# Performance work log

Measured on AMD Instinct MI355X. Metric: run time of the kernel, lower is better.

The kernel has to match this reference:

```python
import jax, jax.numpy as jnp
import numpy as np

N = 100000   # nodes
E = 800000   # directed edges
G = 1000     # graphs
D = 128      # latent_dim
F_IN = 64    # num_node_feats
K = 3        # max_k
BLOCKS = 3   # max_block
H = 5        # multi_h_emb_weight
EPS = 1e-5


def _bn(x, g, b):
    # BatchNorm1d in training mode: biased batch variance
    m = x.mean(axis=0)
    v = x.var(axis=0)
    return (x - m) * jax.lax.rsqrt(v + EPS) * g + b


def setup_inputs() -> dict:
    key = jax.random.key(0)
    ks = jax.random.split(key, 12)
    inp = {
        'node_feat': jax.random.normal(ks[0], (N, F_IN), dtype=jnp.float32),
        'src': jax.random.randint(ks[1], (E,), 0, N),
        'dst': jax.random.randint(ks[2], (E,), 0, N),
        'seg': jnp.sort(jax.random.randint(ks[3], (N,), 0, G)),
        'node_W': jax.random.normal(ks[4], (F_IN, D), dtype=jnp.float32) * 0.05,
        'node_b': jnp.zeros((D,), jnp.float32),
        'bn1_g': jnp.ones((D,), jnp.float32),
        'bn1_b': jnp.zeros((D,), jnp.float32),
        'conv_W': jax.random.normal(ks[5], (K, D, D), dtype=jnp.float32) * 0.05,
        'conv_b': jnp.zeros((K, D), jnp.float32),
        'bn2_g': jnp.ones((K, D), jnp.float32),
        'bn2_b': jnp.zeros((K, D), jnp.float32),
        'k_weight': jax.random.normal(ks[6], (K * D, D), dtype=jnp.float32) * 0.05,
        'bn3_g': jnp.ones((D,), jnp.float32),
        'bn3_b': jnp.zeros((D,), jnp.float32),
        'attn_W1': jax.random.normal(ks[7], (D, D), dtype=jnp.float32) * 0.05,
        'attn_b1': jnp.zeros((D,), jnp.float32),
        'bna_g': jnp.ones((D,), jnp.float32),
        'bna_b': jnp.zeros((D,), jnp.float32),
        'attn_W2': jax.random.normal(ks[8], (D, H), dtype=jnp.float32) * 0.05,
        'attn_b2': jnp.zeros((H,), jnp.float32),
        'bnb_g': jnp.ones((H,), jnp.float32),
        'bnb_b': jnp.zeros((H,), jnp.float32),
    }
    return inp


def reference(node_feat, src, dst, seg,
              node_W, node_b, bn1_g, bn1_b,
              conv_W, conv_b, bn2_g, bn2_b,
              k_weight, bn3_g, bn3_b,
              attn_W1, attn_b1, bna_g, bna_b,
              attn_W2, attn_b2, bnb_g, bnb_b):
    def spmm(x):
        # torch.spmm(A, x) with unweighted n2n adjacency: out[dst] += x[src]
        return jax.ops.segment_sum(x[src], dst, num_segments=N)

    # node embedding: Linear + BN + ReLU
    inp = jax.nn.relu(_bn(node_feat @ node_W + node_b, bn1_g, bn1_b))

    cur = inp
    for block in range(BLOCKS):
        block_input = cur if block == 0 else cur + inp
        # multi_hop: K chained spmm + Linear + BN, concatenated
        input_x = block_input
        outs = []
        for k in range(K):
            pooled = spmm(input_x) + block_input
            input_x = _bn(pooled @ conv_W[k] + conv_b[k], bn2_g[k], bn2_b[k])
            outs.append(input_x)
        result = jnp.concatenate(outs, axis=-1)          # [N, K*D]
        cur = jax.nn.relu(_bn(result @ k_weight, bn3_g, bn3_b))

    node_emb = cur                                       # [N, D]

    # APooling: per-node softmax over heads, segment-wise weighted sum
    a = jnp.tanh(node_emb @ attn_W1 + attn_b1)
    a = _bn(a, bna_g, bna_b)
    a = a @ attn_W2 + attn_b2
    a = _bn(a, bnb_g, bnb_b)                             # [N, H]
    alpha = jax.nn.softmax(a, axis=-1)                   # softmax over head dim (dim=-1)
    # graph_emb[g, h, d] = sum_{n in graph g} alpha[n, h] * node_emb[n, d]
    graph_emb = jax.ops.segment_sum(alpha[:, :, None] * node_emb[:, None, :],
                                    seg, num_segments=G)  # [G, H, D]
    h_out = jax.nn.relu(graph_emb.reshape(G, H * D))

    # L1 regularizer over params with dim > 1, divided by number of graphs
    reg = (jnp.abs(node_W).sum() + jnp.abs(conv_W).sum() + jnp.abs(k_weight).sum()
           + jnp.abs(attn_W1).sum() + jnp.abs(attn_W2).sum())
    return h_out, reg / G
```

## Files before the change

### kernel.cpp

```cpp
#include <hip/hip_runtime.h>
#include <hip/hip_bf16.h>

#define D128 128
#define EPS 1e-5f

typedef unsigned short bfl;
typedef __bf16 bf16x8 __attribute__((ext_vector_type(8)));
typedef float f32x4 __attribute__((ext_vector_type(4)));

__device__ inline float bf2f(unsigned short u) { return __uint_as_float(((unsigned int)u) << 16); }
__device__ inline unsigned short f2bf(float f) {
    unsigned int x = __float_as_uint(f);
    return (unsigned short)((x + 0x7fffu + ((x >> 16) & 1u)) >> 16);
}

__global__ void dag_count_rank(const int* __restrict__ dst, int E,
                               int* __restrict__ deg, int* __restrict__ rank) {
    int i = blockIdx.x * blockDim.x + threadIdx.x;
    int stride = gridDim.x * blockDim.x;
    for (; i < E; i += stride) {
        int r = atomicAdd(&deg[dst[i]], 1);
        rank[i] = r;
    }
}

__global__ void dag_scan1(const int* __restrict__ deg, int N, int* __restrict__ out, int* __restrict__ partials) {
    __shared__ int sdata[256];
    int t = threadIdx.x;
    int base = blockIdx.x * 1024 + t * 4;
    int v[4]; int s = 0;
#pragma unroll
    for (int j = 0; j < 4; j++) { int idx = base + j; v[j] = (idx < N) ? deg[idx] : 0; s += v[j]; }
    sdata[t] = s; __syncthreads();
    for (int off = 1; off < 256; off <<= 1) {
        int x = (t >= off) ? sdata[t - off] : 0;
        __syncthreads();
        sdata[t] += x;
        __syncthreads();
    }
    int run = (t == 0) ? 0 : sdata[t - 1];
#pragma unroll
    for (int j = 0; j < 4; j++) { int idx = base + j; if (idx < N) out[idx] = run; run += v[j]; }
    if (t == 255) partials[blockIdx.x] = sdata[255];
}

__global__ void dag_scan2(int* __restrict__ partials, int P) {
    __shared__ int sdata[256];
    int t = threadIdx.x;
    int v = (t < P) ? partials[t] : 0;
    sdata[t] = v; __syncthreads();
    for (int off = 1; off < 256; off <<= 1) {
        int x = (t >= off) ? sdata[t - off] : 0;
        __syncthreads();
        sdata[t] += x;
        __syncthreads();
    }
    if (t < P) partials[t] = sdata[t] - v;
}

__global__ void dag_scan3(int* __restrict__ rowptr, const int* __restrict__ partials, int N, int E) {
    int i = blockIdx.x * blockDim.x + threadIdx.x;
    int stride = gridDim.x * blockDim.x;
    for (; i < N; i += stride) rowptr[i] += partials[i >> 10];
    if (blockIdx.x == 0 && threadIdx.x == 0) rowptr[N] = E;
}

__global__ void dag_place(const int* __restrict__ src, const int* __restrict__ dst,
                          const int* __restrict__ rank, const int* __restrict__ rowptr,
                          int E, int* __restrict__ csr_src) {
    int i = blockIdx.x * blockDim.x + threadIdx.x;
    int stride = gridDim.x * blockDim.x;
    for (; i < E; i += stride) {
        csr_src[rowptr[dst[i]] + rank[i]] = src[i];
    }
}

__global__ void dag_wconv(const float* __restrict__ node_W, const float* __restrict__ conv_W,
                          const float* __restrict__ k_weight, const float* __restrict__ attn_W1,
                          bfl* __restrict__ wt) {
    int i = blockIdx.x * blockDim.x + threadIdx.x;
    if (i >= 122880) return;
    float v;
    if (i < 8192) {
        int n = i >> 6, k = i & 63;
        v = node_W[k * 128 + n];
    } else if (i < 8192 + 49152) {
        int j = i - 8192; int k = j >> 14; int r = j & 16383;
        int n = r >> 7, kk = r & 127;
        v = conv_W[k * 16384 + kk * 128 + n];
    } else if (i < 8192 + 98304) {
        int j = i - 8192 - 49152; int k = j >> 14; int r = j & 16383;
        int n = r >> 7, kk = r & 127;
        v = k_weight[(k * 128 + kk) * 128 + n];
    } else {
        int j = i - 8192 - 98304;
        int n = j >> 7, kk = j & 127;
        v = attn_W1[kk * 128 + n];
    }
    wt[i] = f2bf(v);
}

template<bool KWPREP>
__global__ void dag_finalize(float* __restrict__ part,
                             const float* __restrict__ g, const float* __restrict__ b,
                             float invN, float* __restrict__ slot,
                             const bfl* __restrict__ WtIn, bfl* __restrict__ Wt2,
                             float* __restrict__ bias2) {
    int t = threadIdx.x;
    float acc = 0.f;
#pragma unroll
    for (int i = 0; i < 8; i++) acc += part[i * 256 + t];
#pragma unroll
    for (int i = 0; i < 8; i++) part[i * 256 + t] = 0.f;
    __shared__ float sums[256];
    __shared__ float scs[128], shs[128];
    sums[t] = acc;
    __syncthreads();
    if (t < 128) {
        float m = sums[t] * invN;
        float var = sums[128 + t] * invN - m * m;
        float scale = g[t] * rsqrtf(var + EPS);
        float shift = b[t] - m * scale;
        scs[t] = scale; shs[t] = shift;
        slot[t] = scale; slot[128 + t] = shift;
    }
    if constexpr (KWPREP) {
        __syncthreads();
        int row = t >> 1, half = t & 1;
        const bfl* wr = WtIn + row * 128 + half * 64;
        bfl* w2 = Wt2 + row * 128 + half * 64;
        float a = 0.f;
        for (int k = 0; k < 64; k += 8) {
            bf16x8 v = *(const bf16x8*)(wr + k);
            bfl o[8];
#pragma unroll
            for (int j = 0; j < 8; j++) {
                float f = (float)v[j];
                int kk = half * 64 + k + j;
                a += shs[kk] * f;
                o[j] = f2bf(scs[kk] * f);
            }
            *(bf16x8*)(w2 + k) = *(bf16x8*)o;
        }
        a += __shfl_xor(a, 1);
        if (half == 0) bias2[row] = a;
    }
}

template<int KSTEPS, int XMODE, bool BIAS, bool TANH, bool ACC, bool STATS>
__global__ __launch_bounds__(256) void gemm_rw(
        const void* __restrict__ Xv, const bfl* __restrict__ Wt,
        const float* __restrict__ bias, bfl* __restrict__ Y,
        int Nrows, float* __restrict__ partOut) {
    const int Kdim = KSTEPS * 32;
    int t = threadIdx.x;
    int lane = t & 63;
    int wave = t >> 6;
    int cg = wave & 1, rg = wave >> 1;
    int l15 = lane & 15, lg = lane >> 4;

    bf16x8 af[4][KSTEPS];
#pragma unroll
    for (int nf = 0; nf < 4; nf++)
#pragma unroll
        for (int ks = 0; ks < KSTEPS; ks++)
            af[nf][ks] = *(const bf16x8*)(Wt + (size_t)(cg * 64 + nf * 16 + l15) * Kdim + ks * 32 + lg * 8);

    float bia[4][4];
    if (BIAS) {
#pragma unroll
        for (int nf = 0; nf < 4; nf++) {
            float4 bb = *(const float4*)(bias + cg * 64 + nf * 16 + lg * 4);
            bia[nf][0] = bb.x; bia[nf][1] = bb.y; bia[nf][2] = bb.z; bia[nf][3] = bb.w;
        }
    }

    float s_c[4][4], q_c[4][4];
    if constexpr (STATS) {
#pragma unroll
        for (int nf = 0; nf < 4; nf++)
#pragma unroll
            for (int j = 0; j < 4; j++) { s_c[nf][j] = 0.f; q_c[nf][j] = 0.f; }
    }

    const int RT = (Nrows + 15) >> 4;
    const int step = gridDim.x * 2;

    auto load_bf = [&](int rt, bf16x8* bfo) {
        int r = rt * 16 + l15;
        bool valid = (rt < RT) && (r < Nrows);
#pragma unroll
        for (int ks = 0; ks < KSTEPS; ks++) {
            if (valid) {
                if (XMODE == 0) {
                    bfo[ks] = *(const bf16x8*)((const bfl*)Xv + (size_t)r * Kdim + ks * 32 + lg * 8);
                } else {
                    const float* xp = (const float*)Xv + (size_t)r * Kdim + ks * 32 + lg * 8;
                    float4 a4 = *(const float4*)xp;
                    float4 b4 = *(const float4*)(xp + 4);
                    bf16x8 bb;
                    bb[0] = (__bf16)a4.x; bb[1] = (__bf16)a4.y; bb[2] = (__bf16)a4.z; bb[3] = (__bf16)a4.w;
                    bb[4] = (__bf16)b4.x; bb[5] = (__bf16)b4.y; bb[6] = (__bf16)b4.z; bb[7] = (__bf16)b4.w;
                    bfo[ks] = bb;
                }
            } else {
                bf16x8 bb;
#pragma unroll
                for (int j = 0; j < 8; j++) bb[j] = (__bf16)0.f;
                bfo[ks] = bb;
            }
        }
    };

    auto compute_store = [&](int rt, const bf16x8* bfc) {
        int r = rt * 16 + l15;
        bool valid = (rt < RT) && (r < Nrows);
        f32x4 acc[4];
#pragma unroll
        for (int nf = 0; nf < 4; nf++) acc[nf] = (f32x4)0.f;
#pragma unroll
        for (int ks = 0; ks < KSTEPS; ks++)
#pragma unroll
            for (int nf = 0; nf < 4; nf++)
                acc[nf] = __builtin_amdgcn_mfma_f32_16x16x32_bf16(af[nf][ks], bfc[ks], acc[nf], 0, 0, 0);
#pragma unroll
        for (int nf = 0; nf < 4; nf++) {
            int c0 = cg * 64 + nf * 16 + lg * 4;
            f32x4 v = acc[nf];
            if (BIAS) {
#pragma unroll
                for (int j = 0; j < 4; j++) v[j] += bia[nf][j];
            }
            if (TANH) {
#pragma unroll
                for (int j = 0; j < 4; j++) v[j] = tanhf(v[j]);
            }
            if (valid) {
                bfl* yp = Y + (size_t)r * D128 + c0;
                if (ACC) {
                    ushort4 old = *(const ushort4*)yp;
                    v[0] += bf2f(old.x); v[1] += bf2f(old.y); v[2] += bf2f(old.z); v[3] += bf2f(old.w);
                }
                ushort4 o;
                o.x = f2bf(v[0]); o.y = f2bf(v[1]); o.z = f2bf(v[2]); o.w = f2bf(v[3]);
                *(ushort4*)yp = o;
            }
            if constexpr (STATS) {
#pragma unroll
                for (int j = 0; j < 4; j++) {
                    float f = valid ? v[j] : 0.f;
                    s_c[nf][j] += f;
                    q_c[nf][j] += f * f;
                }
            }
        }
    };

    for (int rt = blockIdx.x * 2 + rg; rt < RT; rt += 2 * step) {
        bf16x8 bfA[KSTEPS], bfB[KSTEPS];
        load_bf(rt, bfA);
        load_bf(rt + step, bfB);
        compute_store(rt, bfA);
        compute_store(rt + step, bfB);
    }

    if constexpr (STATS) {
#pragma unroll
        for (int nf = 0; nf < 4; nf++)
#pragma unroll
            for (int j = 0; j < 4; j++) {
                float s = s_c[nf][j], q = q_c[nf][j];
                s += __shfl_xor(s, 1); s += __shfl_xor(s, 2); s += __shfl_xor(s, 4); s += __shfl_xor(s, 8);
                q += __shfl_xor(q, 1); q += __shfl_xor(q, 2); q += __shfl_xor(q, 4); q += __shfl_xor(q, 8);
                s_c[nf][j] = s; q_c[nf][j] = q;
            }
        __shared__ float red[2][2][64];
        ((float*)red)[t] = 0.f;
        __syncthreads();
        if (l15 == 0) {
#pragma unroll
            for (int nf = 0; nf < 4; nf++)
#pragma unroll
                for (int j = 0; j < 4; j++) {
                    int c = nf * 16 + lg * 4 + j;
                    atomicAdd(&red[cg][0][c], s_c[nf][j]);
                    atomicAdd(&red[cg][1][c], q_c[nf][j]);
                }
        }
        __syncthreads();
        int cgi = t >> 7, stat = (t >> 6) & 1, c = t & 63;
        atomicAdd(&partOut[(size_t)(blockIdx.x & 7) * 256 + stat * 128 + cgi * 64 + c],
                  red[cgi][stat][c]);
    }
}

__global__ __launch_bounds__(256) void dag_spmm(
        const bfl* __restrict__ x, const bfl* __restrict__ bi,
        const int* __restrict__ rowptr, const int* __restrict__ csr_src,
        bfl* __restrict__ out, int N, const float* __restrict__ scsh) {
    int lane = threadIdx.x & 63;
    int n = blockIdx.x * 4 + (threadIdx.x >> 6);
    if (n >= N) return;
    int c0 = lane * 2;
    float sc0 = 1.f, sc1 = 1.f, sh0 = 0.f, sh1 = 0.f;
    if (scsh) {
        sc0 = scsh[c0];     sh0 = scsh[128 + c0];
        sc1 = scsh[c0 + 1]; sh1 = scsh[128 + c0 + 1];
    }
    int p0 = rowptr[n], p1 = rowptr[n + 1];
    unsigned int ub = *(const unsigned int*)(bi + (size_t)n * D128 + c0);
    const bfl* xb = x + c0;
    float ax[8], ay[8];
#pragma unroll
    for (int j = 0; j < 8; j++) { ax[j] = 0.f; ay[j] = 0.f; }
    int p = p0;
    for (; p + 8 <= p1; p += 8) {
        unsigned int u[8];
#pragma unroll
        for (int j = 0; j < 8; j++) {
            int s = csr_src[p + j];
            u[j] = *(const unsigned int*)(xb + (size_t)s * D128);
        }
#pragma unroll
        for (int j = 0; j < 8; j++) {
            ax[j] += __uint_as_float(u[j] << 16);
            ay[j] += __uint_as_float(u[j] & 0xffff0000u);
        }
    }
    {
        int rem = p1 - p;
        unsigned int u[8];
#pragma unroll
        for (int j = 0; j < 8; j++) {
            if (j < rem) {
                int s = csr_src[p + j];
                u[j] = *(const unsigned int*)(xb + (size_t)s * D128);
            }
        }
#pragma unroll
        for (int j = 0; j < 8; j++) {
            if (j < rem) {
                ax[j] += __uint_as_float(u[j] << 16);
                ay[j] += __uint_as_float(u[j] & 0xffff0000u);
            }
        }
    }
    float vx = ((ax[0] + ax[1]) + (ax[2] + ax[3])) + ((ax[4] + ax[5]) + (ax[6] + ax[7]));
    float vy = ((ay[0] + ay[1]) + (ay[2] + ay[3])) + ((ay[4] + ay[5]) + (ay[6] + ay[7]));
    float cnt = (float)(p1 - p0);
    vx = sc0 * vx + cnt * sh0 + __uint_as_float(ub << 16);
    vy = sc1 * vy + cnt * sh1 + __uint_as_float(ub & 0xffff0000u);
    unsigned int uo = (unsigned int)f2bf(vx) | ((unsigned int)f2bf(vy) << 16);
    *(unsigned int*)(out + (size_t)n * D128 + c0) = uo;
}

__global__ void dag_colstat_f32(const float* __restrict__ Y, int Nrows, int C, float* __restrict__ sums) {
    __shared__ float ls[8], lss[8];
    int t = threadIdx.x;
    int nlanes = blockDim.x / C;
    int col = t % C, lane = t / C;
    float s = 0.f, ss = 0.f;
    if (lane < nlanes) {
        for (int r = blockIdx.x * nlanes + lane; r < Nrows; r += gridDim.x * nlanes) {
            float v = Y[(size_t)r * C + col];
            s += v; ss += v * v;
        }
    }
    if (t < C) { ls[t] = 0.f; lss[t] = 0.f; }
    __syncthreads();
    if (lane < nlanes) { atomicAdd(&ls[col], s); atomicAdd(&lss[col], ss); }
    __syncthreads();
    if (t < C) { atomicAdd(&sums[t], ls[t]); atomicAdd(&sums[C + t], lss[t]); }
}

template<bool RELU, bool ADDOUT>
__global__ void dag_bn_apply(bfl* __restrict__ Y, const float* __restrict__ scsh,
                             size_t n8,
                             const bfl* __restrict__ addin, bfl* __restrict__ out2) {
    __shared__ float sc[128], sh[128];
    int t = threadIdx.x;
    if (t < 128) {
        sc[t] = scsh[t];
        sh[t] = scsh[128 + t];
    }
    __syncthreads();
    for (size_t i = (size_t)blockIdx.x * blockDim.x + t; i < n8; i += (size_t)gridDim.x * blockDim.x) {
        int c0 = (int)((i * 8) & 127);
        bf16x8 v = *(bf16x8*)(Y + i * 8);
        bfl o[8], o2[8];
#pragma unroll
        for (int j = 0; j < 8; j++) {
            float f = (float)v[j] * sc[c0 + j] + sh[c0 + j];
            if (RELU) f = fmaxf(f, 0.f);
            o[j] = f2bf(f);
            if (ADDOUT) o2[j] = f2bf(f + bf2f(addin[i * 8 + j]));
        }
        *(bf16x8*)(Y + i * 8) = *(bf16x8*)o;
        if (ADDOUT) *(bf16x8*)(out2 + i * 8) = *(bf16x8*)o2;
    }
}

__global__ void dag_gemm5(const bfl* __restrict__ X, const float* __restrict__ W,
                          const float* __restrict__ bias, float* __restrict__ Y, int Nrows,
                          const float* __restrict__ scsh) {
    __shared__ float Xs[32][132];
    __shared__ float Ws[640];
    __shared__ float sc[128], sh[128];
    int t = threadIdx.x;
    if (t < 128) {
        sc[t] = scsh[t];
        sh[t] = scsh[128 + t];
    }
    for (int i = t; i < 640; i += 256) Ws[i] = W[i];
    __syncthreads();
    int row0 = blockIdx.x * 32;
#pragma unroll
    for (int i = 0; i < 2; i++) {
        int off = (i * 256 + t) * 8;
        int r = off >> 7, c = off & 127;
        int gr = row0 + r;
        if (gr < Nrows) {
            bf16x8 v = *(const bf16x8*)(X + (size_t)gr * D128 + c);
#pragma unroll
            for (int j = 0; j < 8; j++) Xs[r][c + j] = (float)v[j] * sc[c + j] + sh[c + j];
        } else {
#pragma unroll
            for (int j = 0; j < 8; j++) Xs[r][c + j] = 0.f;
        }
    }
    __syncthreads();
    if (t < 160) {
        int r = t / 5, h = t % 5;
        int gr = row0 + r;
        if (gr < Nrows) {
            float s = bias[h];
            for (int k = 0; k < 128; k++) s = fmaf(Xs[r][k], Ws[k * 5 + h], s);
            Y[(size_t)gr * 5 + h] = s;
        }
    }
}

__global__ void dag_alpha(float* __restrict__ a2, int N,
                          const float* __restrict__ sums, const float* __restrict__ g,
                          const float* __restrict__ b, float invN) {
    float scb[5], shb[5];
#pragma unroll
    for (int h = 0; h < 5; h++) {
        float s = sums[h], ss = sums[5 + h];
        float m = s * invN;
        float var = ss * invN - m * m;
        float scale = g[h] * rsqrtf(var + EPS);
        scb[h] = scale; shb[h] = b[h] - m * scale;
    }
    int n = blockIdx.x * blockDim.x + threadIdx.x;
    if (n >= N) return;
    float av[5];
    float mx = -1e30f;
#pragma unroll
    for (int h = 0; h < 5; h++) {
        av[h] = a2[(size_t)n * 5 + h] * scb[h] + shb[h];
        mx = fmaxf(mx, av[h]);
    }
    float s = 0.f;
#pragma unroll
    for (int h = 0; h < 5; h++) { av[h] = expf(av[h] - mx); s += av[h]; }
    float inv = 1.f / s;
#pragma unroll
    for (int h = 0; h < 5; h++) a2[(size_t)n * 5 + h] = av[h] * inv;
}

__global__ void dag_pool(const float* __restrict__ alpha, const bfl* __restrict__ emb,
                         const int* __restrict__ seg, int N, int G, float* __restrict__ out) {
    int gg = blockIdx.x;
    int d = threadIdx.x;
    int lo = 0, hi = N;
    while (lo < hi) { int m = (lo + hi) >> 1; if (seg[m] < gg) lo = m + 1; else hi = m; }
    int start = lo;
    lo = start; hi = N;
    while (lo < hi) { int m = (lo + hi) >> 1; if (seg[m] < gg + 1) lo = m + 1; else hi = m; }
    int end = lo;
    float acc[5] = {0.f, 0.f, 0.f, 0.f, 0.f};
    for (int n = start; n < end; n++) {
        float e = bf2f(emb[(size_t)n * D128 + d]);
#pragma unroll
        for (int h = 0; h < 5; h++) acc[h] = fmaf(alpha[(size_t)n * 5 + h], e, acc[h]);
    }
#pragma unroll
    for (int h = 0; h < 5; h++) out[(size_t)gg * 640 + h * D128 + d] = fmaxf(acc[h], 0.f);
}

__global__ void dag_reg(const float* w0, int n0, const float* w1, int n1, const float* w2, int n2,
                        const float* w3, int n3, const float* w4, int n4, float* out, float invG) {
    __shared__ float sd[256];
    int t = threadIdx.x;
    int gt = blockIdx.x * blockDim.x + t;
    int stride = gridDim.x * blockDim.x;
    float s = 0.f;
    const float* ws[5] = {w0, w1, w2, w3, w4};
    int ns[5] = {n0, n1, n2, n3, n4};
    for (int a = 0; a < 5; a++) {
        const float* w = ws[a]; int n = ns[a];
        for (int i = gt; i < n; i += stride) s += fabsf(w[i]);
    }
    sd[t] = s; __syncthreads();
    for (int off = 128; off > 0; off >>= 1) { if (t < off) sd[t] += sd[t + off]; __syncthreads(); }
    if (t == 0) atomicAdd(out, sd[0] * invG);
}

extern "C" void kernel_launch(void* const* d_in, const int* in_sizes, int n_in,
                              void* d_out, int out_size, void* d_ws, size_t ws_size,
                              hipStream_t stream) {
    const float* node_feat = (const float*)d_in[0];
    const int*   src       = (const int*)d_in[1];
    const int*   dst       = (const int*)d_in[2];
    const int*   seg       = (const int*)d_in[3];
    const float* node_W    = (const float*)d_in[4];
    const float* node_b    = (const float*)d_in[5];
    const float* bn1_g     = (const float*)d_in[6];
    const float* bn1_b     = (const float*)d_in[7];
    const float* conv_W    = (const float*)d_in[8];
    const float* conv_b    = (const float*)d_in[9];
    const float* bn2_g     = (const float*)d_in[10];
    const float* bn2_b     = (const float*)d_in[11];
    const float* k_weight  = (const float*)d_in[12];
    const float* bn3_g     = (const float*)d_in[13];
    const float* bn3_b     = (const float*)d_in[14];
    const float* attn_W1   = (const float*)d_in[15];
    const float* attn_b1   = (const float*)d_in[16];
    const float* bna_g     = (const float*)d_in[17];
    const float* bna_b     = (const float*)d_in[18];
    const float* attn_W2   = (const float*)d_in[19];
    const float* attn_b2   = (const float*)d_in[20];
    const float* bnb_g     = (const float*)d_in[21];
    const float* bnb_b     = (const float*)d_in[22];

    const int N = in_sizes[3];
    const int E = in_sizes[1];
    const int G = (out_size - 1) / 640;
    const int FIN = in_sizes[0] / N;
    const float invN = 1.f / (float)N;

    auto align256 = [](size_t x) { return (x + 255) & ~(size_t)255; };
    size_t NB = (size_t)N * D128 * sizeof(bfl);
    char* w = (char*)d_ws;
    bfl* P0 = (bfl*)(w + 0 * NB);
    bfl* P1 = (bfl*)(w + 1 * NB);
    bfl* P2 = (bfl*)(w + 2 * NB);
    bfl* P3 = (bfl*)(w + 3 * NB);
    bfl* P4 = (bfl*)(w + 4 * NB);
    char* tail = w + 5 * NB;
    size_t off = 0;
    int gemmGrid = (N + 127) / 128;
    float* stats = (float*)(tail + off); off = align256(off + 15 * 256 * sizeof(float));
    float* part  = (float*)(tail + off); off = align256(off + 8 * 256 * sizeof(float));
    bfl*   wt    = (bfl*)(tail + off);   off = align256(off + 122880 * sizeof(bfl));
    bfl*   wt2   = (bfl*)(tail + off);   off = align256(off + 16384 * sizeof(bfl));
    float* bias2 = (float*)(tail + off); off = align256(off + 128 * sizeof(float));
    float* a2    = (float*)(tail + off); off = align256(off + (size_t)N * 5 * sizeof(float));
    int* deg     = (int*)(tail + off);   off = align256(off + (size_t)N * 4);
    int* rowptr  = (int*)(tail + off);   off = align256(off + (size_t)(N + 1) * 4);
    int* rank    = (int*)(tail + off);   off = align256(off + (size_t)E * 4);
    int* csr_src = (int*)(tail + off);   off = align256(off + (size_t)E * 4);
    int* partials= (int*)(tail + off);   off = align256(off + 512);

    bfl* wt_node = wt;
    bfl* wt_conv = wt + 8192;
    bfl* wt_kw   = wt + 8192 + 49152;
    bfl* wt_attn = wt + 8192 + 98304;
    auto slot = [&](int s) { return stats + (size_t)s * 256; };

    int spmmGrid = (N + 3) / 4;

    hipMemsetAsync(part, 0, 8 * 256 * sizeof(float), stream);
    hipMemsetAsync(slot(14), 0, 256 * sizeof(float), stream);
    hipMemsetAsync((float*)d_out + (size_t)G * 640, 0, 4, stream);

    hipMemsetAsync(deg, 0, (size_t)N * 4, stream);
    dag_count_rank<<<1024, 256, 0, stream>>>(dst, E, deg, rank);
    int P = (N + 1023) / 1024;
    dag_scan1<<<P, 256, 0, stream>>>(deg, N, rowptr, partials);
    dag_scan2<<<1, 256, 0, stream>>>(partials, P);
    dag_scan3<<<256, 256, 0, stream>>>(rowptr, partials, N, E);
    dag_place<<<1024, 256, 0, stream>>>(src, dst, rank, rowptr, E, csr_src);

    dag_wconv<<<480, 256, 0, stream>>>(node_W, conv_W, k_weight, attn_W1, wt);

    dag_reg<<<64, 256, 0, stream>>>(node_W, FIN * D128, conv_W, 3 * D128 * D128,
                                    k_weight, 3 * D128 * D128, attn_W1, D128 * D128,
                                    attn_W2, D128 * 5, (float*)d_out + (size_t)G * 640, 1.0f / G);

    gemm_rw<2, 1, true, false, false, true><<<gemmGrid, 256, 0, stream>>>(
        node_feat, wt_node, node_b, P0, N, part);
    dag_finalize<false><<<1, 256, 0, stream>>>(part, bn1_g, bn1_b, invN,
                                               slot(0), nullptr, nullptr, nullptr);
    dag_bn_apply<true, false><<<2048, 256, 0, stream>>>(P0, slot(0), (size_t)N * D128 / 8,
                                                        nullptr, nullptr);

    for (int blk = 0; blk < 3; blk++) {
        const bfl* bip = (blk == 0) ? P0 : P1;
        for (int k = 0; k < 3; k++) {
            int s2i = 1 + blk * 3 + k;
            const bfl* in_x = (k == 0) ? bip : P4;
            const float* s2 = (k == 0) ? nullptr : slot(s2i - 1);
            dag_spmm<<<spmmGrid, 256, 0, stream>>>(in_x, bip, rowptr, csr_src, P3, N, s2);
            gemm_rw<4, 0, true, false, false, true><<<gemmGrid, 256, 0, stream>>>(
                P3, wt_conv + (size_t)k * 16384, conv_b + k * D128, P4, N, part);
            dag_finalize<true><<<1, 256, 0, stream>>>(part,
                                                      bn2_g + k * D128, bn2_b + k * D128, invN,
                                                      slot(s2i), wt_kw + (size_t)k * 16384, wt2, bias2);
            if (k == 0)
                gemm_rw<4, 0, true, false, false, false><<<gemmGrid, 256, 0, stream>>>(
                    P4, wt2, bias2, P2, N, nullptr);
            else if (k == 1)
                gemm_rw<4, 0, true, false, true, false><<<gemmGrid, 256, 0, stream>>>(
                    P4, wt2, bias2, P2, N, nullptr);
            else
                gemm_rw<4, 0, true, false, true, true><<<gemmGrid, 256, 0, stream>>>(
                    P4, wt2, bias2, P2, N, part);
        }
        dag_finalize<false><<<1, 256, 0, stream>>>(part, bn3_g, bn3_b, invN,
                                                   slot(10 + blk), nullptr, nullptr, nullptr);
        if (blk < 2)
            dag_bn_apply<true, true><<<2048, 256, 0, stream>>>(P2, slot(10 + blk),
                                                               (size_t)N * D128 / 8, P0, P1);
        else
            dag_bn_apply<true, false><<<2048, 256, 0, stream>>>(P2, slot(10 + blk),
                                                                (size_t)N * D128 / 8, nullptr, nullptr);
    }

    gemm_rw<4, 0, true, true, false, true><<<gemmGrid, 256, 0, stream>>>(
        P2, wt_attn, attn_b1, P3, N, part);
    dag_finalize<false><<<1, 256, 0, stream>>>(part, bna_g, bna_b, invN,
                                               slot(13), nullptr, nullptr, nullptr);
    dag_gemm5<<<(N + 31) / 32, 256, 0, stream>>>(P3, attn_W2, attn_b2, a2, N, slot(13));
    dag_colstat_f32<<<256, 255, 0, stream>>>(a2, N, 5, slot(14));
    dag_alpha<<<(N + 255) / 256, 256, 0, stream>>>(a2, N, slot(14), bnb_g, bnb_b, invN);
    dag_pool<<<G, 128, 0, stream>>>(a2, P2, seg, N, G, (float*)d_out);
}
```

Before: 1.244 ms.

## Widen SpMM gathers to 16-byte loads and skip dead BN write

The SpMM kernel now maps 16 lanes to each node row, so each lane gathers 8 bf16 values with one 16-byte load, and a wave handles 4 nodes instead of one. The loop runs to the maximum degree among the 4 nodes and predicates the lanes whose node has fewer edges. This aims to cut per-edge memory instructions and raise memory-level parallelism for the neighbour gather, at the cost of divergence when degrees differ. Separately, the BN-apply for blocks 0 and 1 no longer writes the normalized result back to P2, since only the residual output P1 is consumed afterwards, which saves one full activation write per block.

Measured after the change: 1.158 ms. 1.07x faster.

```diff
diff --git a/kernel.cpp b/kernel.cpp
--- a/kernel.cpp
+++ b/kernel.cpp
@@ -298,60 +298,85 @@
         const bfl* __restrict__ x, const bfl* __restrict__ bi,
         const int* __restrict__ rowptr, const int* __restrict__ csr_src,
         bfl* __restrict__ out, int N, const float* __restrict__ scsh) {
-    int lane = threadIdx.x & 63;
-    int n = blockIdx.x * 4 + (threadIdx.x >> 6);
-    if (n >= N) return;
-    int c0 = lane * 2;
-    float sc0 = 1.f, sc1 = 1.f, sh0 = 0.f, sh1 = 0.f;
+    int t = threadIdx.x;
+    int lane = t & 63;
+    int wave = t >> 6;
+    int l16 = lane & 15;
+    int sub = lane >> 4;
+    int c0 = l16 * 8;
+    int n = blockIdx.x * 16 + wave * 4 + sub;
+    bool valid = n < N;
+
+    float sc[8], sh[8];
     if (scsh) {
-        sc0 = scsh[c0];     sh0 = scsh[128 + c0];
-        sc1 = scsh[c0 + 1]; sh1 = scsh[128 + c0 + 1];
-    }
-    int p0 = rowptr[n], p1 = rowptr[n + 1];
-    unsigned int ub = *(const unsigned int*)(bi + (size_t)n * D128 + c0);
+        float4 a = *(const float4*)(scsh + c0);
+        float4 b = *(const float4*)(scsh + c0 + 4);
+        float4 p = *(const float4*)(scsh + 128 + c0);
+        float4 q = *(const float4*)(scsh + 128 + c0 + 4);
+        sc[0] = a.x; sc[1] = a.y; sc[2] = a.z; sc[3] = a.w;
+        sc[4] = b.x; sc[5] = b.y; sc[6] = b.z; sc[7] = b.w;
+        sh[0] = p.x; sh[1] = p.y; sh[2] = p.z; sh[3] = p.w;
+        sh[4] = q.x; sh[5] = q.y; sh[6] = q.z; sh[7] = q.w;
+    } else {
+#pragma unroll
+        for (int j = 0; j < 8; j++) { sc[j] = 1.f; sh[j] = 0.f; }
+    }
+
+    int p0 = valid ? rowptr[n] : 0;
+    int p1 = valid ? rowptr[n + 1] : 0;
+    int deg = p1 - p0;
+    int md = deg;
+    md = max(md, __shfl_xor(md, 16));
+    md = max(md, __shfl_xor(md, 32));
+
+    uint4 ub = make_uint4(0, 0, 0, 0);
+    if (valid) ub = *(const uint4*)(bi + (size_t)n * D128 + c0);
+
     const bfl* xb = x + c0;
-    float ax[8], ay[8];
-#pragma unroll
-    for (int j = 0; j < 8; j++) { ax[j] = 0.f; ay[j] = 0.f; }
-    int p = p0;
-    for (; p + 8 <= p1; p += 8) {
-        unsigned int u[8];
-#pragma unroll
-        for (int j = 0; j < 8; j++) {
-            int s = csr_src[p + j];
-            u[j] = *(const unsigned int*)(xb + (size_t)s * D128);
-        }
-#pragma unroll
-        for (int j = 0; j < 8; j++) {
-            ax[j] += __uint_as_float(u[j] << 16);
-            ay[j] += __uint_as_float(u[j] & 0xffff0000u);
-        }
-    }
-    {
-        int rem = p1 - p;
-        unsigned int u[8];
-#pragma unroll
-        for (int j = 0; j < 8; j++) {
-            if (j < rem) {
-                int s = csr_src[p + j];
-                u[j] = *(const unsigned int*)(xb + (size_t)s * D128);
-            }
-        }
-#pragma unroll
-        for (int j = 0; j < 8; j++) {
-            if (j < rem) {
-                ax[j] += __uint_as_float(u[j] << 16);
-                ay[j] += __uint_as_float(u[j] & 0xffff0000u);
-            }
-        }
-    }
-    float vx = ((ax[0] + ax[1]) + (ax[2] + ax[3])) + ((ax[4] + ax[5]) + (ax[6] + ax[7]));
-    float vy = ((ay[0] + ay[1]) + (ay[2] + ay[3])) + ((ay[4] + ay[5]) + (ay[6] + ay[7]));
-    float cnt = (float)(p1 - p0);
-    vx = sc0 * vx + cnt * sh0 + __uint_as_float(ub << 16);
-    vy = sc1 * vy + cnt * sh1 + __uint_as_float(ub & 0xffff0000u);
-    unsigned int uo = (unsigned int)f2bf(vx) | ((unsigned int)f2bf(vy) << 16);
-    *(unsigned int*)(out + (size_t)n * D128 + c0) = uo;
+    float acc[8];
+#pragma unroll
+    for (int j = 0; j < 8; j++) acc[j] = 0.f;
+
+    for (int j = 0; j < md; j += 4) {
+        uint4 u[4];
+#pragma unroll
+        for (int r = 0; r < 4; r++) {
+            u[r] = make_uint4(0, 0, 0, 0);
+            if (j + r < deg) {
+                int s = csr_src[p0 + j + r];
+                u[r] = *(const uint4*)(xb + (size_t)s * D128);
+            }
+        }
+#pragma unroll
+        for (int r = 0; r < 4; r++) {
+            acc[0] += __uint_as_float(u[r].x << 16);
+            acc[1] += __uint_as_float(u[r].x & 0xffff0000u);
+            acc[2] += __uint_as_float(u[r].y << 16);
+            acc[3] += __uint_as_float(u[r].y & 0xffff0000u);
+            acc[4] += __uint_as_float(u[r].z << 16);
+            acc[5] += __uint_as_float(u[r].z & 0xffff0000u);
+            acc[6] += __uint_as_float(u[r].w << 16);
+            acc[7] += __uint_as_float(u[r].w & 0xffff0000u);
+        }
+    }
+
+    if (valid) {
+        float cnt = (float)deg;
+        float bv[8];
+        bv[0] = __uint_as_float(ub.x << 16); bv[1] = __uint_as_float(ub.x & 0xffff0000u);
+        bv[2] = __uint_as_float(ub.y << 16); bv[3] = __uint_as_float(ub.y & 0xffff0000u);
+        bv[4] = __uint_as_float(ub.z << 16); bv[5] = __uint_as_float(ub.z & 0xffff0000u);
+        bv[6] = __uint_as_float(ub.w << 16); bv[7] = __uint_as_float(ub.w & 0xffff0000u);
+        float v[8];
+#pragma unroll
+        for (int j = 0; j < 8; j++) v[j] = sc[j] * acc[j] + cnt * sh[j] + bv[j];
+        uint4 o;
+        o.x = (unsigned int)f2bf(v[0]) | ((unsigned int)f2bf(v[1]) << 16);
+        o.y = (unsigned int)f2bf(v[2]) | ((unsigned int)f2bf(v[3]) << 16);
+        o.z = (unsigned int)f2bf(v[4]) | ((unsigned int)f2bf(v[5]) << 16);
+        o.w = (unsigned int)f2bf(v[6]) | ((unsigned int)f2bf(v[7]) << 16);
+        *(uint4*)(out + (size_t)n * D128 + c0) = o;
+    }
 }
 
 __global__ void dag_colstat_f32(const float* __restrict__ Y, int Nrows, int C, float* __restrict__ sums) {
@@ -373,7 +398,7 @@
     if (t < C) { atomicAdd(&sums[t], ls[t]); atomicAdd(&sums[C + t], lss[t]); }
 }
 
-template<bool RELU, bool ADDOUT>
+template<bool RELU, bool ADDOUT, bool WRITEY>
 __global__ void dag_bn_apply(bfl* __restrict__ Y, const float* __restrict__ scsh,
                              size_t n8,
                              const bfl* __restrict__ addin, bfl* __restrict__ out2) {
@@ -395,7 +420,7 @@
             o[j] = f2bf(f);
             if (ADDOUT) o2[j] = f2bf(f + bf2f(addin[i * 8 + j]));
         }
-        *(bf16x8*)(Y + i * 8) = *(bf16x8*)o;
+        if (WRITEY) *(bf16x8*)(Y + i * 8) = *(bf16x8*)o;
         if (ADDOUT) *(bf16x8*)(out2 + i * 8) = *(bf16x8*)o2;
     }
 }
@@ -569,7 +594,7 @@
     bfl* wt_attn = wt + 8192 + 98304;
     auto slot = [&](int s) { return stats + (size_t)s * 256; };
 
-    int spmmGrid = (N + 3) / 4;
+    int spmmGrid = (N + 15) / 16;
 
     hipMemsetAsync(part, 0, 8 * 256 * sizeof(float), stream);
     hipMemsetAsync(slot(14), 0, 256 * sizeof(float), stream);
@@ -593,8 +618,8 @@
         node_feat, wt_node, node_b, P0, N, part);
     dag_finalize<false><<<1, 256, 0, stream>>>(part, bn1_g, bn1_b, invN,
                                                slot(0), nullptr, nullptr, nullptr);
-    dag_bn_apply<true, false><<<2048, 256, 0, stream>>>(P0, slot(0), (size_t)N * D128 / 8,
-                                                        nullptr, nullptr);
+    dag_bn_apply<true, false, true><<<2048, 256, 0, stream>>>(P0, slot(0), (size_t)N * D128 / 8,
+                                                              nullptr, nullptr);
 
     for (int blk = 0; blk < 3; blk++) {
         const bfl* bip = (blk == 0) ? P0 : P1;
@@ -621,11 +646,11 @@
         dag_finalize<false><<<1, 256, 0, stream>>>(part, bn3_g, bn3_b, invN,
                                                    slot(10 + blk), nullptr, nullptr, nullptr);
         if (blk < 2)
-            dag_bn_apply<true, true><<<2048, 256, 0, stream>>>(P2, slot(10 + blk),
-                                                               (size_t)N * D128 / 8, P0, P1);
+            dag_bn_apply<true, true, false><<<2048, 256, 0, stream>>>(P2, slot(10 + blk),
+                                                                      (size_t)N * D128 / 8, P0, P1);
         else
-            dag_bn_apply<true, false><<<2048, 256, 0, stream>>>(P2, slot(10 + blk),
-                                                                (size_t)N * D128 / 8, nullptr, nullptr);
+            dag_bn_apply<true, false, true><<<2048, 256, 0, stream>>>(P2, slot(10 + blk),
+                                                                      (size_t)N * D128 / 8, nullptr, nullptr);
     }
 
     gemm_rw<4, 0, true, true, false, true><<<gemmGrid, 256, 0, stream>>>(
```
